# Kernel optimization log

Measured on AMD Instinct MI355X. Metric: run time of the kernel, lower is better.

The kernel has to match this reference:

```python
import jax, jax.numpy as jnp
import numpy as np

N_NODES = 100000
N_EDGES = 1600000
IN_FEATS = 256
OUT_FEATS = 128
GAMMA = 1.0


def setup_inputs() -> dict:
    key = jax.random.key(0)
    k1, k2, k3, k4, k5 = jax.random.split(key, 5)
    glorot = np.sqrt(6.0 / (IN_FEATS + OUT_FEATS)).astype(np.float32)
    feat = jax.random.normal(k1, (N_NODES, IN_FEATS), dtype=jnp.float32)
    W_mean = jax.random.uniform(k2, (IN_FEATS, OUT_FEATS), dtype=jnp.float32, minval=-glorot, maxval=glorot)
    W_var = jax.random.uniform(k3, (IN_FEATS, OUT_FEATS), dtype=jnp.float32, minval=-glorot, maxval=glorot)
    src = jax.random.randint(k4, (N_EDGES,), 0, N_NODES, dtype=jnp.int64 if jax.config.jax_enable_x64 else jnp.int32)
    dst = jax.random.randint(k5, (N_EDGES,), 0, N_NODES, dtype=jnp.int64 if jax.config.jax_enable_x64 else jnp.int32)
    return {"feat": feat, "W_mean": W_mean, "W_var": W_var, "src": src, "dst": dst}


def reference(feat, W_mean, W_var, src, dst):
    # dense projections + relu (no bias, as bias=False)
    mean = jax.nn.relu(jnp.matmul(feat, W_mean))   # [N, F]
    var = jax.nn.relu(jnp.matmul(feat, W_var))     # [N, F]
    attention = jnp.exp(-GAMMA * var)
    # in-degrees from dst edge endpoints, clamped to >= 1
    degs = jax.ops.segment_sum(jnp.ones_like(dst, dtype=jnp.float32), dst, num_segments=N_NODES)
    degs = jnp.clip(degs, 1.0)
    norm1 = (degs ** -0.5)[:, None]                # [N, 1] = D^{-1/2}
    norm2 = norm1 * norm1                          # [N, 1] = D^{-1}
    m_msg = mean * attention * norm1
    v_msg = var * attention * attention * norm2
    # copy_src + sum aggregation (SpMM over edge list)
    mean_agg = jax.ops.segment_sum(m_msg[src], dst, num_segments=N_NODES) * norm1
    var_agg = jax.ops.segment_sum(v_msg[src], dst, num_segments=N_NODES) * norm2
    return mean_agg, var_agg
```

## Files before the change

kernel.cpp:

```cpp
#include <hip/hip_runtime.h>
#include <hip/hip_bf16.h>

#define N_NODES 100000
#define N_EDGES 1600000
#define OUTF 128
#define INF 256
#define SCAN_CHUNK 1024
#define SCAN_BLOCKS 98
#define M_TILES 6250

typedef _Float16 f16;
typedef _Float16 half8 __attribute__((ext_vector_type(8)));
typedef _Float16 half4 __attribute__((ext_vector_type(4)));
typedef _Float16 half2v __attribute__((ext_vector_type(2)));
typedef float floatx4 __attribute__((ext_vector_type(4)));

__global__ void count_rank_kernel(const int* __restrict__ dst, int E,
                                  int* __restrict__ deg, int* __restrict__ rank) {
    int i = blockIdx.x * blockDim.x + threadIdx.x;
    if (i < E) rank[i] = atomicAdd(&deg[dst[i]], 1);
}

__global__ __launch_bounds__(256) void scan_partial_kernel(const int* __restrict__ deg, int n,
                                                           int* __restrict__ partial) {
    __shared__ int red[256];
    int b = blockIdx.x, t = threadIdx.x;
    int base = b * SCAN_CHUNK;
    int s = 0;
    for (int i = t; i < SCAN_CHUNK; i += 256) {
        int idx = base + i;
        if (idx < n) s += deg[idx];
    }
    red[t] = s;
    __syncthreads();
    for (int off = 128; off > 0; off >>= 1) {
        if (t < off) red[t] += red[t + off];
        __syncthreads();
    }
    if (t == 0) partial[b] = red[0];
}

__global__ __launch_bounds__(128) void scan_top_kernel(int* __restrict__ partial, int nb,
                                                       int* __restrict__ row_start, int n) {
    __shared__ int sc[128];
    int t = threadIdx.x;
    int v = (t < nb) ? partial[t] : 0;
    sc[t] = v;
    __syncthreads();
    for (int off = 1; off < 128; off <<= 1) {
        int val = sc[t];
        int add = (t >= off) ? sc[t - off] : 0;
        __syncthreads();
        sc[t] = val + add;
        __syncthreads();
    }
    if (t < nb) partial[t] = sc[t] - v;
    if (t == 127) row_start[n] = sc[127];
}

__global__ __launch_bounds__(256) void scan_final_kernel(const int* __restrict__ deg, int n,
                                                         const int* __restrict__ partial,
                                                         int* __restrict__ row_start,
                                                         float* __restrict__ norm1,
                                                         float* __restrict__ norm2) {
    __shared__ int sc[256];
    int b = blockIdx.x, t = threadIdx.x;
    int base = b * SCAN_CHUNK + t * 4;
    int v[4];
    int tsum = 0;
#pragma unroll
    for (int j = 0; j < 4; j++) {
        int idx = base + j;
        v[j] = (idx < n) ? deg[idx] : 0;
        tsum += v[j];
    }
    sc[t] = tsum;
    __syncthreads();
    for (int off = 1; off < 256; off <<= 1) {
        int val = sc[t];
        int add = (t >= off) ? sc[t - off] : 0;
        __syncthreads();
        sc[t] = val + add;
        __syncthreads();
    }
    int run = sc[t] - tsum + partial[b];
#pragma unroll
    for (int j = 0; j < 4; j++) {
        int idx = base + j;
        if (idx < n) {
            row_start[idx] = run;
            float d = (float)(v[j] > 0 ? v[j] : 1);
            norm1[idx] = rsqrtf(d);
            norm2[idx] = 1.0f / d;
            run += v[j];
        }
    }
}

__global__ void scatter_edges_kernel(const int* __restrict__ src, const int* __restrict__ dst,
                                     const int* __restrict__ rank,
                                     const int* __restrict__ row_start,
                                     int E, int* __restrict__ srcs_sorted) {
    int i = blockIdx.x * blockDim.x + threadIdx.x;
    if (i < E) {
        srcs_sorted[row_start[dst[i]] + rank[i]] = src[i];
    }
}

__global__ __launch_bounds__(256) void convert_B_kernel(const float* __restrict__ Wm,
                                                        const float* __restrict__ Wv,
                                                        f16* __restrict__ Bt) {
    int k = threadIdx.x;
    int ng = blockIdx.x;
    int g = ng >> 4, i = ng & 15;
    int ch = g >> 3, w = (g >> 1) & 3, cg = g & 1;
    int col = ch * 64 + w * 16 + i;
    const float* srcW = cg ? Wv : Wm;
    Bt[ng * 256 + k] = (f16)srcW[k * 128 + col];
}

__global__ __launch_bounds__(256, 3) void proj_mfma_kernel(const float* __restrict__ feat,
                                                           const f16* __restrict__ Bt,
                                                           const float* __restrict__ norm1,
                                                           const float* __restrict__ norm2,
                                                           f16* __restrict__ msg) {
    __shared__ float As[2][16 * 256];

    int tid = threadIdx.x;
    int w = tid >> 6;
    int lane = tid & 63;
    int quad = lane >> 4;
    int l15 = lane & 15;

    int bidx = blockIdx.x;
    int jj, ch;
    if (bidx < 2496) {
        jj = (bidx >> 4) * 8 + (bidx & 7);
        ch = (bidx >> 3) & 1;
    } else {
        int r = bidx - 2496;
        jj = 1248 + (r >> 1);
        ch = r & 1;
    }
    int tbase = jj;

    half8 b[2][8];
#pragma unroll
    for (int cg = 0; cg < 2; cg++) {
        int g = ch * 8 + w * 2 + cg;
        const f16* bp = Bt + (size_t)(g * 16 + l15) * 256 + quad * 8;
#pragma unroll
        for (int kf = 0; kf < 8; kf++) {
            b[cg][kf] = *(const half8*)(bp + kf * 32);
        }
    }
#pragma unroll
    for (int cg = 0; cg < 2; cg++) {
#pragma unroll
        for (int kf = 0; kf < 8; kf++) {
            asm volatile("" : "+v"(b[cg][kf]));
        }
    }

    int col = ch * 64 + w * 16 + l15;

    int swz = (l15 & 7) << 4;
    int rb0 = l15 * 1024 + ((quad * 32) ^ swz);
    int rb1 = l15 * 1024 + ((quad * 32 + 16) ^ swz);

    int lsw = lane * 16;

    auto stage = [&](int buf, int t) {
        int m0 = t * 16;
#pragma unroll
        for (int j = 0; j < 4; j++) {
            int r = w * 4 + j;
            const char* gp = (const char*)(feat + (size_t)(m0 + r) * 256)
                             + (lsw ^ ((r & 7) << 4));
            char* lp = (char*)&As[buf][0] + r * 1024;
            __builtin_amdgcn_global_load_lds(
                (const __attribute__((address_space(1))) void*)gp,
                (__attribute__((address_space(3))) void*)lp, 16, 0, 0);
        }
    };

    stage(0, tbase);
    int cur = 0;

    for (int t = tbase; t < M_TILES; t += 1250) {
        __syncthreads();

        int tn = t + 1250;
        if (tn < M_TILES) stage(cur ^ 1, tn);

        const char* ab = (const char*)&As[cur][0];
        half8 a[8];
#pragma unroll
        for (int kf = 0; kf < 8; kf++) {
            floatx4 f0 = *(const floatx4*)(ab + rb0 + kf * 128);
            floatx4 f1 = *(const floatx4*)(ab + rb1 + kf * 128);
            half8 h;
            h[0] = (f16)f0.x; h[1] = (f16)f0.y; h[2] = (f16)f0.z; h[3] = (f16)f0.w;
            h[4] = (f16)f1.x; h[5] = (f16)f1.y; h[6] = (f16)f1.z; h[7] = (f16)f1.w;
            a[kf] = h;
        }

        int m0 = t * 16;
        float s1r[4], s2r[4];
#pragma unroll
        for (int r = 0; r < 4; r++) {
            int node = m0 + quad * 4 + r;
            s1r[r] = norm1[node];
            s2r[r] = norm2[node];
        }

        floatx4 acc0 = (floatx4){0.f, 0.f, 0.f, 0.f};
        floatx4 acc1 = (floatx4){0.f, 0.f, 0.f, 0.f};
#pragma unroll
        for (int kf = 0; kf < 8; kf++) {
            acc0 = __builtin_amdgcn_mfma_f32_16x16x32_f16(a[kf], b[0][kf], acc0, 0, 0, 0);
            acc1 = __builtin_amdgcn_mfma_f32_16x16x32_f16(a[kf], b[1][kf], acc1, 0, 0, 0);
        }

#pragma unroll
        for (int r = 0; r < 4; r++) {
            int node = m0 + quad * 4 + r;
            float m = fmaxf(acc0[r], 0.f);
            float v = fmaxf(acc1[r], 0.f);
            float att = __expf(-v);
            half2v pr;
            pr[0] = (f16)(m * att * s1r[r]);
            pr[1] = (f16)(v * att * att * s2r[r]);
            *(half2v*)(msg + (size_t)node * 256 + col * 2) = pr;
        }
        cur ^= 1;
    }
}

__global__ __launch_bounds__(256) void agg_kernel(const int* __restrict__ row_start,
                                                  const int* __restrict__ srcs,
                                                  const f16* __restrict__ msg,
                                                  const float* __restrict__ norm1,
                                                  const float* __restrict__ norm2,
                                                  float* __restrict__ out_mean,
                                                  float* __restrict__ out_var) {
    int d = blockIdx.x * 4 + (threadIdx.x >> 6);
    int lane = threadIdx.x & 63;
    int half = lane >> 5;
    int j = lane & 31;

    int s0 = row_start[d];
    int s1 = row_start[d + 1];

    float am0 = 0.f, am1 = 0.f, am2 = 0.f, am3 = 0.f;
    float av0 = 0.f, av1 = 0.f, av2 = 0.f, av3 = 0.f;

    int i = s0 + half;
    for (; i + 6 < s1; i += 8) {
        int sa = srcs[i], sb = srcs[i + 2], sc = srcs[i + 4], sd = srcs[i + 6];
        half8 ha = *(const half8*)(msg + (size_t)sa * 256 + j * 8);
        half8 hb = *(const half8*)(msg + (size_t)sb * 256 + j * 8);
        half8 hc = *(const half8*)(msg + (size_t)sc * 256 + j * 8);
        half8 hd = *(const half8*)(msg + (size_t)sd * 256 + j * 8);
        am0 += (float)ha[0] + (float)hb[0] + (float)hc[0] + (float)hd[0];
        av0 += (float)ha[1] + (float)hb[1] + (float)hc[1] + (float)hd[1];
        am1 += (float)ha[2] + (float)hb[2] + (float)hc[2] + (float)hd[2];
        av1 += (float)ha[3] + (float)hb[3] + (float)hc[3] + (float)hd[3];
        am2 += (float)ha[4] + (float)hb[4] + (float)hc[4] + (float)hd[4];
        av2 += (float)ha[5] + (float)hb[5] + (float)hc[5] + (float)hd[5];
        am3 += (float)ha[6] + (float)hb[6] + (float)hc[6] + (float)hd[6];
        av3 += (float)ha[7] + (float)hb[7] + (float)hc[7] + (float)hd[7];
    }
    for (; i < s1; i += 2) {
        int sa = srcs[i];
        half8 ha = *(const half8*)(msg + (size_t)sa * 256 + j * 8);
        am0 += (float)ha[0];
        av0 += (float)ha[1];
        am1 += (float)ha[2];
        av1 += (float)ha[3];
        am2 += (float)ha[4];
        av2 += (float)ha[5];
        am3 += (float)ha[6];
        av3 += (float)ha[7];
    }

    am0 += __shfl_xor(am0, 32, 64);
    am1 += __shfl_xor(am1, 32, 64);
    am2 += __shfl_xor(am2, 32, 64);
    am3 += __shfl_xor(am3, 32, 64);
    av0 += __shfl_xor(av0, 32, 64);
    av1 += __shfl_xor(av1, 32, 64);
    av2 += __shfl_xor(av2, 32, 64);
    av3 += __shfl_xor(av3, 32, 64);

    if (half == 0) {
        float k1 = norm1[d], k2 = norm2[d];
        floatx4 om = {am0 * k1, am1 * k1, am2 * k1, am3 * k1};
        floatx4 ov = {av0 * k2, av1 * k2, av2 * k2, av3 * k2};
        __builtin_nontemporal_store(om, (floatx4*)(out_mean + (size_t)d * 128 + j * 4));
        __builtin_nontemporal_store(ov, (floatx4*)(out_var + (size_t)d * 128 + j * 4));
    }
}

extern "C" void kernel_launch(void* const* d_in, const int* in_sizes, int n_in,
                              void* d_out, int out_size, void* d_ws, size_t ws_size,
                              hipStream_t stream) {
    const float* feat = (const float*)d_in[0];
    const float* Wm = (const float*)d_in[1];
    const float* Wv = (const float*)d_in[2];
    const int* src = (const int*)d_in[3];
    const int* dst = (const int*)d_in[4];
    float* out = (float*)d_out;

    const int N = N_NODES;
    const int E = N_EDGES;

    char* wsp = (char*)d_ws;
    auto carve = [&](size_t bytes) {
        char* p = wsp;
        wsp += (bytes + 255) & ~(size_t)255;
        return p;
    };
    f16* msg = (f16*)carve((size_t)N * 256 * sizeof(f16));
    f16* Bt = (f16*)carve((size_t)256 * 256 * sizeof(f16));
    int* srcs_sorted = (int*)carve((size_t)E * 4);
    int* rank = (int*)carve((size_t)E * 4);
    int* deg = (int*)carve((size_t)N * 4);
    int* row_start = (int*)carve((size_t)(N + 1) * 4);
    float* norm1 = (float*)carve((size_t)N * 4);
    float* norm2 = (float*)carve((size_t)N * 4);
    int* partial = (int*)carve(128 * 4);

    hipMemsetAsync(deg, 0, (size_t)N * 4, stream);

    count_rank_kernel<<<(E + 255) / 256, 256, 0, stream>>>(dst, E, deg, rank);
    convert_B_kernel<<<256, 256, 0, stream>>>(Wm, Wv, Bt);
    scan_partial_kernel<<<SCAN_BLOCKS, 256, 0, stream>>>(deg, N, partial);
    scan_top_kernel<<<1, 128, 0, stream>>>(partial, SCAN_BLOCKS, row_start, N);
    scan_final_kernel<<<SCAN_BLOCKS, 256, 0, stream>>>(deg, N, partial, row_start, norm1, norm2);
    scatter_edges_kernel<<<(E + 255) / 256, 256, 0, stream>>>(src, dst, rank, row_start, E,
                                                              srcs_sorted);
    proj_mfma_kernel<<<2500, 256, 0, stream>>>(feat, Bt, norm1, norm2, msg);
    agg_kernel<<<N / 4, 256, 0, stream>>>(row_start, srcs_sorted, msg, norm1, norm2,
                                          out, out + (size_t)N * OUTF);
}
```

Baseline: 430.1 us.

## Fuse degree count with weight conversion and edge scatter with projection kernel

```diff
diff --git a/kernel.cpp b/kernel.cpp
--- a/kernel.cpp
+++ b/kernel.cpp
@@ -9,16 +9,47 @@
 #define SCAN_BLOCKS 98
 #define M_TILES 6250
 
+#define CNT_BLOCKS 1563
+#define PROJ_BLOCKS 2500
+#define SCAT_BLOCKS 1563
+
 typedef _Float16 f16;
 typedef _Float16 half8 __attribute__((ext_vector_type(8)));
 typedef _Float16 half4 __attribute__((ext_vector_type(4)));
 typedef _Float16 half2v __attribute__((ext_vector_type(2)));
 typedef float floatx4 __attribute__((ext_vector_type(4)));
 
-__global__ void count_rank_kernel(const int* __restrict__ dst, int E,
-                                  int* __restrict__ deg, int* __restrict__ rank) {
-    int i = blockIdx.x * blockDim.x + threadIdx.x;
-    if (i < E) rank[i] = atomicAdd(&deg[dst[i]], 1);
+__global__ void count_convB_kernel(const int* __restrict__ dst, int E,
+                                   int* __restrict__ deg, int* __restrict__ rank,
+                                   const float* __restrict__ Wm,
+                                   const float* __restrict__ Wv,
+                                   f16* __restrict__ Bt) {
+    int bid = blockIdx.x;
+    if (bid >= CNT_BLOCKS) {
+        int ng = bid - CNT_BLOCKS;
+        int k = threadIdx.x;
+        int g = ng >> 4, i = ng & 15;
+        int ch = g >> 3, w = (g >> 1) & 3, cg = g & 1;
+        int col = ch * 64 + w * 16 + i;
+        const float* srcW = cg ? Wv : Wm;
+        Bt[ng * 256 + k] = (f16)srcW[k * 128 + col];
+        return;
+    }
+    int e0 = bid * 1024 + threadIdx.x * 4;
+    if (e0 + 3 < E) {
+        int4 d4 = *(const int4*)(dst + e0);
+        int4 r4;
+        r4.x = atomicAdd(&deg[d4.x], 1);
+        r4.y = atomicAdd(&deg[d4.y], 1);
+        r4.z = atomicAdd(&deg[d4.z], 1);
+        r4.w = atomicAdd(&deg[d4.w], 1);
+        *(int4*)(rank + e0) = r4;
+    } else {
+        for (int j = 0; j < 4; j++) {
+            int e = e0 + j;
+            if (e < E) rank[e] = atomicAdd(&deg[dst[e]], 1);
+        }
+    }
 }
 
 __global__ __launch_bounds__(256) void scan_partial_kernel(const int* __restrict__ deg, int n,
@@ -97,52 +128,51 @@
     }
 }
 
-__global__ void scatter_edges_kernel(const int* __restrict__ src, const int* __restrict__ dst,
-                                     const int* __restrict__ rank,
-                                     const int* __restrict__ row_start,
-                                     int E, int* __restrict__ srcs_sorted) {
-    int i = blockIdx.x * blockDim.x + threadIdx.x;
-    if (i < E) {
-        srcs_sorted[row_start[dst[i]] + rank[i]] = src[i];
-    }
-}
-
-__global__ __launch_bounds__(256) void convert_B_kernel(const float* __restrict__ Wm,
-                                                        const float* __restrict__ Wv,
-                                                        f16* __restrict__ Bt) {
-    int k = threadIdx.x;
-    int ng = blockIdx.x;
-    int g = ng >> 4, i = ng & 15;
-    int ch = g >> 3, w = (g >> 1) & 3, cg = g & 1;
-    int col = ch * 64 + w * 16 + i;
-    const float* srcW = cg ? Wv : Wm;
-    Bt[ng * 256 + k] = (f16)srcW[k * 128 + col];
-}
-
-__global__ __launch_bounds__(256, 3) void proj_mfma_kernel(const float* __restrict__ feat,
-                                                           const f16* __restrict__ Bt,
-                                                           const float* __restrict__ norm1,
-                                                           const float* __restrict__ norm2,
-                                                           f16* __restrict__ msg) {
+__global__ __launch_bounds__(256, 3) void proj_scatter_kernel(
+        const float* __restrict__ feat, const f16* __restrict__ Bt,
+        const float* __restrict__ norm1, const float* __restrict__ norm2,
+        f16* __restrict__ msg,
+        const int* __restrict__ src, const int* __restrict__ dst,
+        const int* __restrict__ rank, const int* __restrict__ row_start,
+        int E, int* __restrict__ srcs_sorted) {
     __shared__ float As[2][16 * 256];
+
+    int bid = blockIdx.x;
+    int rr = bid % 13, q = bid / 13;
+    int proj_id = -1, scat_id = -1;
+    if (rr < 8) {
+        proj_id = q * 8 + rr;
+        if (proj_id >= PROJ_BLOCKS) { scat_id = 1560 + (proj_id - PROJ_BLOCKS); proj_id = -1; }
+    } else {
+        scat_id = q * 5 + (rr - 8);
+    }
+
+    if (scat_id >= 0) {
+        int e0 = scat_id * 1024 + threadIdx.x * 4;
+        if (e0 + 3 < E) {
+            int4 s4 = *(const int4*)(src + e0);
+            int4 d4 = *(const int4*)(dst + e0);
+            int4 r4 = *(const int4*)(rank + e0);
+            srcs_sorted[row_start[d4.x] + r4.x] = s4.x;
+            srcs_sorted[row_start[d4.y] + r4.y] = s4.y;
+            srcs_sorted[row_start[d4.z] + r4.z] = s4.z;
+            srcs_sorted[row_start[d4.w] + r4.w] = s4.w;
+        } else {
+            for (int j = 0; j < 4; j++) {
+                int e = e0 + j;
+                if (e < E) srcs_sorted[row_start[dst[e]] + rank[e]] = src[e];
+            }
+        }
+        return;
+    }
 
     int tid = threadIdx.x;
     int w = tid >> 6;
     int lane = tid & 63;
     int quad = lane >> 4;
     int l15 = lane & 15;
-
-    int bidx = blockIdx.x;
-    int jj, ch;
-    if (bidx < 2496) {
-        jj = (bidx >> 4) * 8 + (bidx & 7);
-        ch = (bidx >> 3) & 1;
-    } else {
-        int r = bidx - 2496;
-        jj = 1248 + (r >> 1);
-        ch = r & 1;
-    }
-    int tbase = jj;
+    int ch = proj_id & 1;
+    int tbase = proj_id >> 1;
 
     half8 b[2][8];
 #pragma unroll
@@ -167,7 +197,6 @@
     int swz = (l15 & 7) << 4;
     int rb0 = l15 * 1024 + ((quad * 32) ^ swz);
     int rb1 = l15 * 1024 + ((quad * 32 + 16) ^ swz);
-
     int lsw = lane * 16;
 
     auto stage = [&](int buf, int t) {
@@ -333,14 +362,12 @@
 
     hipMemsetAsync(deg, 0, (size_t)N * 4, stream);
 
-    count_rank_kernel<<<(E + 255) / 256, 256, 0, stream>>>(dst, E, deg, rank);
-    convert_B_kernel<<<256, 256, 0, stream>>>(Wm, Wv, Bt);
+    count_convB_kernel<<<CNT_BLOCKS + 256, 256, 0, stream>>>(dst, E, deg, rank, Wm, Wv, Bt);
     scan_partial_kernel<<<SCAN_BLOCKS, 256, 0, stream>>>(deg, N, partial);
     scan_top_kernel<<<1, 128, 0, stream>>>(partial, SCAN_BLOCKS, row_start, N);
     scan_final_kernel<<<SCAN_BLOCKS, 256, 0, stream>>>(deg, N, partial, row_start, norm1, norm2);
-    scatter_edges_kernel<<<(E + 255) / 256, 256, 0, stream>>>(src, dst, rank, row_start, E,
-                                                              srcs_sorted);
-    proj_mfma_kernel<<<2500, 256, 0, stream>>>(feat, Bt, norm1, norm2, msg);
+    proj_scatter_kernel<<<PROJ_BLOCKS + SCAT_BLOCKS, 256, 0, stream>>>(
+        feat, Bt, norm1, norm2, msg, src, dst, rank, row_start, E, srcs_sorted);
     agg_kernel<<<N / 4, 256, 0, stream>>>(row_start, srcs_sorted, msg, norm1, norm2,
                                           out, out + (size_t)N * OUTF);
 }
```

Result: faster. 412.3 us (-4.1%).
